# Performance work log

Measured on AMD Instinct MI355X. Metric: run time of the kernel, lower is better.

Reference implementation:

```python
import jax, jax.numpy as jnp
import numpy as np

N_NODES = 50000
N_EDGES = 800000
D_IN = 96
D_OUT = 96
K_ORDER = 3


def setup_inputs() -> dict:
    key = jax.random.key(0)
    k1, k2, k3, k4, k5 = jax.random.split(key, 5)
    rows = jax.random.randint(k1, (N_EDGES,), 0, N_NODES, dtype=jnp.int64 if jax.config.jax_enable_x64 else jnp.int32)
    cols = jax.random.randint(k2, (N_EDGES,), 0, N_NODES, dtype=jnp.int64 if jax.config.jax_enable_x64 else jnp.int32)
    vals = jax.random.uniform(k3, (N_EDGES,), dtype=jnp.float32) * (1.0 / 16.0)  # ~sym-normalized weights
    H = jax.random.normal(k4, (N_NODES, D_IN), dtype=jnp.float32)
    W = jax.random.normal(k5, (D_IN, D_OUT), dtype=jnp.float32) * (1.0 / np.sqrt(D_IN))
    bias = jnp.zeros((D_OUT,), dtype=jnp.float32)
    return {"rows": rows, "cols": cols, "vals": vals, "H": H, "W": W, "bias": bias}


def reference(rows, cols, vals, H, W, bias):
    n = H.shape[0]

    def spmm(X):  # L @ X via gather-multiply-scatter over COO edges
        return jax.ops.segment_sum(vals[:, None] * X[cols], rows, num_segments=n)

    def ln_mm(X):  # (2L - I) @ X
        return 2.0 * spmm(X) - X

    # k = 0 term: T_0 = H
    H_out = H @ W
    # k = 1 term: T_1 = (2L - I) H  (differentiable, as in torch code)
    T_prev = H
    T_curr = ln_mm(H)
    H_out = H_out + T_curr @ W
    # k >= 2: recurrence computed under no_grad in the original -> stop_gradient
    for _ in range(2, K_ORDER + 1):
        T_next = jax.lax.stop_gradient(2.0 * ln_mm(T_curr) - T_prev)
        H_out = H_out + T_next @ W
        T_prev, T_curr = T_curr, T_next
    return H_out + bias
```

## Files before the change

kernel.cpp:

```cpp
#include <hip/hip_runtime.h>
#include <hip/hip_fp16.h>

#define NN 50000
#define NE 800000
#define D  96
#define NB_SCAN 196
#define N4 (NN * D / 4)
#define CB4 ((N4 + 255) / 256)
#define WFRAG_BLKS 5

typedef unsigned int   uint32;
typedef unsigned short uint16;
typedef short  v8s __attribute__((ext_vector_type(8)));
typedef float  v4f __attribute__((ext_vector_type(4)));
typedef unsigned int v2u __attribute__((ext_vector_type(2)));
typedef unsigned int v4u __attribute__((ext_vector_type(4)));

__device__ inline uint16 f32_to_bf16(float f) {
    uint32 u = __float_as_uint(f);
    u += 0x7FFF + ((u >> 16) & 1);
    return (uint16)(u >> 16);
}

__device__ inline void u2f(v2u u, float& a, float& b, float& c, float& d) {
    a = __uint_as_float(u.x << 16);
    b = __uint_as_float(u.x & 0xFFFF0000u);
    c = __uint_as_float(u.y << 16);
    d = __uint_as_float(u.y & 0xFFFF0000u);
}

__device__ inline float f16_val(uint32 e) {
    __half_raw h; h.x = (uint16)(e >> 16);
    return __half2float(__half(h));
}

__device__ inline uint32 comb2(uint32 u1, uint32 u2, uint32 u3) {
    float a1 = __uint_as_float(u1 << 16), b1 = __uint_as_float(u1 & 0xFFFF0000u);
    float a2 = __uint_as_float(u2 << 16), b2 = __uint_as_float(u2 & 0xFFFF0000u);
    float a3 = __uint_as_float(u3 << 16), b3 = __uint_as_float(u3 & 0xFFFF0000u);
    float sa = 12.f * a1 - 40.f * a2 + 32.f * a3;
    float sb = 12.f * b1 - 40.f * b2 + 32.f * b3;
    return (uint32)f32_to_bf16(sa) | ((uint32)f32_to_bf16(sb) << 16);
}

__global__ void prep(const float4* __restrict__ H, ushort4* __restrict__ Hb,
                     const float* __restrict__ W, uint16* __restrict__ Wfrag,
                     int* __restrict__ counts) {
    int b = blockIdx.x;
    int t = threadIdx.x;
    if (b < CB4) {
        int i = b * 256 + t;
        if (i < N4) {
            float4 v = H[i];
            ushort4 o;
            o.x = f32_to_bf16(v.x); o.y = f32_to_bf16(v.y);
            o.z = f32_to_bf16(v.z); o.w = f32_to_bf16(v.w);
            Hb[i] = o;
        }
    } else if (b < CB4 + NB_SCAN) {
        int i = (b - CB4) * 256 + t;
        if (i < NN) counts[i] = 0;
    } else {
        int idx = (b - CB4 - NB_SCAN) * 256 + t;
        if (idx < 18 * 64) {
            int bt = idx >> 6, lane = idx & 63;
            int nt = bt / 3, kc = bt % 3;
            int col = nt * 16 + (lane & 15);
            int kbase = kc * 32 + (lane >> 4) * 8;
            uint16 tmp[8];
            #pragma unroll
            for (int j = 0; j < 8; ++j) tmp[j] = f32_to_bf16(W[(kbase + j) * D + col]);
            uint32* dst = (uint32*)(Wfrag + ((size_t)bt * 64 + lane) * 8);
            const uint32* src = (const uint32*)tmp;
            #pragma unroll
            for (int j = 0; j < 4; ++j) dst[j] = src[j];
        }
    }
}

__global__ void hist_slots(const int* __restrict__ rows, int* __restrict__ counts,
                           int* __restrict__ slot) {
    int e = blockIdx.x * blockDim.x + threadIdx.x;
    if (e < NE) slot[e] = atomicAdd(&counts[rows[e]], 1);
}

__global__ void scan_p1(const int* __restrict__ counts, int* __restrict__ partials) {
    __shared__ int red[256];
    int t = threadIdx.x;
    int i = blockIdx.x * 256 + t;
    red[t] = (i < NN) ? counts[i] : 0;
    __syncthreads();
    for (int off = 128; off > 0; off >>= 1) {
        if (t < off) red[t] += red[t + off];
        __syncthreads();
    }
    if (t == 0) partials[blockIdx.x] = red[0];
}

__global__ void scan_p23(const int* __restrict__ counts, const int* __restrict__ partials,
                         int* __restrict__ row_ptr) {
    __shared__ int pp[256];
    __shared__ int sh[256];
    int t = threadIdx.x;
    pp[t] = (t < NB_SCAN) ? partials[t] : 0;
    __syncthreads();
    for (int off = 1; off < 256; off <<= 1) {
        int u = (t >= off) ? pp[t - off] : 0;
        __syncthreads();
        pp[t] += u;
        __syncthreads();
    }
    int blk_off = (blockIdx.x == 0) ? 0 : pp[blockIdx.x - 1];
    int i = blockIdx.x * 256 + t;
    int v = (i < NN) ? counts[i] : 0;
    sh[t] = v;
    __syncthreads();
    for (int off = 1; off < 256; off <<= 1) {
        int u = (t >= off) ? sh[t - off] : 0;
        __syncthreads();
        sh[t] += u;
        __syncthreads();
    }
    int excl = sh[t] - v + blk_off;
    if (i < NN) row_ptr[i] = excl;
    if (i == NN - 1) row_ptr[NN] = excl + v;
}

__global__ void fill_edges(const int* __restrict__ rows, const int* __restrict__ cols,
                           const float* __restrict__ vals, const int* __restrict__ row_ptr,
                           const int* __restrict__ slot, uint32* __restrict__ edges) {
    int e = blockIdx.x * blockDim.x + threadIdx.x;
    if (e < NE) {
        int p = row_ptr[rows[e]] + slot[e];
        __half_raw hr = __half_raw(__float2half(vals[e]));
        edges[p] = (uint32)(cols[e] & 0xFFFF) | ((uint32)hr.x << 16);
    }
}

__global__ void spmm(const int* __restrict__ row_ptr, const uint32* __restrict__ edges,
                     const uint16* __restrict__ Xb, uint16* __restrict__ Yb) {
    int tid  = threadIdx.x;
    int lane = tid & 31;
    int g    = tid >> 5;
    int r = blockIdx.x * 8 + g;
    if (r >= NN) return;
    if (lane >= 24) return;

    const v2u* xbase = (const v2u*)Xb;

    float ax = 0.f, ay = 0.f, az = 0.f, aw = 0.f;

    int s = row_ptr[r];
    int e = row_ptr[r + 1];
    int i = s;
    for (; i + 7 < e; i += 8) {
        uint32 ee[8];
        #pragma unroll
        for (int j = 0; j < 8; ++j) ee[j] = edges[i + j];
        v2u xx[8];
        #pragma unroll
        for (int j = 0; j < 8; ++j)
            xx[j] = xbase[(size_t)(ee[j] & 0xFFFF) * 24 + lane];
        #pragma unroll
        for (int j = 0; j < 8; ++j) {
            float v = f16_val(ee[j]);
            float x0,x1,x2,x3;
            u2f(xx[j], x0,x1,x2,x3);
            ax += v*x0; ay += v*x1; az += v*x2; aw += v*x3;
        }
    }
    for (; i + 3 < e; i += 4) {
        uint32 ee[4];
        #pragma unroll
        for (int j = 0; j < 4; ++j) ee[j] = edges[i + j];
        v2u xx[4];
        #pragma unroll
        for (int j = 0; j < 4; ++j)
            xx[j] = xbase[(size_t)(ee[j] & 0xFFFF) * 24 + lane];
        #pragma unroll
        for (int j = 0; j < 4; ++j) {
            float v = f16_val(ee[j]);
            float x0,x1,x2,x3;
            u2f(xx[j], x0,x1,x2,x3);
            ax += v*x0; ay += v*x1; az += v*x2; aw += v*x3;
        }
    }
    for (; i < e; ++i) {
        uint32 e0 = edges[i];
        float v = f16_val(e0);
        v2u x = xbase[(size_t)(e0 & 0xFFFF) * 24 + lane];
        float x0,x1,x2,x3;
        u2f(x, x0,x1,x2,x3);
        ax += v*x0; ay += v*x1; az += v*x2; aw += v*x3;
    }

    v2u o;
    o.x = (uint32)f32_to_bf16(ax) | ((uint32)f32_to_bf16(ay) << 16);
    o.y = (uint32)f32_to_bf16(az) | ((uint32)f32_to_bf16(aw) << 16);
    __builtin_nontemporal_store(o, (v2u*)(Yb + (size_t)r * D) + lane);
}

__global__ void mfma_gemm(const uint16* __restrict__ U1, const uint16* __restrict__ U2,
                          const uint16* __restrict__ U3, const uint16* __restrict__ Wfrag,
                          const float* __restrict__ bias, float* __restrict__ out) {
    int tid   = threadIdx.x;
    int lane  = tid & 63;
    int wv    = blockIdx.x * (blockDim.x >> 6) + (tid >> 6);
    int nwv   = gridDim.x * (blockDim.x >> 6);
    int col   = lane & 15;
    int quad  = lane >> 4;

    v8s wf[6][3];
    #pragma unroll
    for (int nt = 0; nt < 6; ++nt)
        #pragma unroll
        for (int kc = 0; kc < 3; ++kc)
            wf[nt][kc] = ((const v8s*)Wfrag)[(nt * 3 + kc) * 64 + lane];

    float bi[6];
    #pragma unroll
    for (int nt = 0; nt < 6; ++nt) bi[nt] = bias[nt * 16 + col];

    for (int s = wv; s < NN / 16; s += nwv) {
        int r0 = s * 16;
        size_t base = (size_t)(r0 + col) * D + quad * 8;
        v8s a[3];
        #pragma unroll
        for (int kc = 0; kc < 3; ++kc) {
            v4u u1 = *(const v4u*)(U1 + base + kc * 32);
            v4u u2 = *(const v4u*)(U2 + base + kc * 32);
            v4u u3 = *(const v4u*)(U3 + base + kc * 32);
            v4u sres;
            #pragma unroll
            for (int j = 0; j < 4; ++j) sres[j] = comb2(u1[j], u2[j], u3[j]);
            a[kc] = __builtin_bit_cast(v8s, sres);
        }
        v4f acc[6];
        #pragma unroll
        for (int nt = 0; nt < 6; ++nt) {
            v4f c = {0.f, 0.f, 0.f, 0.f};
            c = __builtin_amdgcn_mfma_f32_16x16x32_bf16(a[0], wf[nt][0], c, 0, 0, 0);
            c = __builtin_amdgcn_mfma_f32_16x16x32_bf16(a[1], wf[nt][1], c, 0, 0, 0);
            c = __builtin_amdgcn_mfma_f32_16x16x32_bf16(a[2], wf[nt][2], c, 0, 0, 0);
            acc[nt] = c;
        }
        #pragma unroll
        for (int nt = 0; nt < 6; ++nt) {
            float* o = out + (size_t)(r0 + quad * 4) * D + nt * 16 + col;
            o[0 * D] = acc[nt][0] + bi[nt];
            o[1 * D] = acc[nt][1] + bi[nt];
            o[2 * D] = acc[nt][2] + bi[nt];
            o[3 * D] = acc[nt][3] + bi[nt];
        }
    }
}

extern "C" void kernel_launch(void* const* d_in, const int* in_sizes, int n_in,
                              void* d_out, int out_size, void* d_ws, size_t ws_size,
                              hipStream_t stream) {
    const int*   rows = (const int*)d_in[0];
    const int*   cols = (const int*)d_in[1];
    const float* vals = (const float*)d_in[2];
    const float* H    = (const float*)d_in[3];
    const float* W    = (const float*)d_in[4];
    const float* bias = (const float*)d_in[5];
    float* out = (float*)d_out;

    char* ws = (char*)d_ws;
    uint16* Hb       = (uint16*)ws;  ws += (size_t)NN * D * 2;
    uint16* U1b      = (uint16*)ws;  ws += (size_t)NN * D * 2;
    uint16* U2b      = (uint16*)ws;  ws += (size_t)NN * D * 2;
    uint16* U3b      = (uint16*)ws;  ws += (size_t)NN * D * 2;
    uint32* edges    = (uint32*)ws;  ws += (size_t)NE * 4;
    uint16* Wfrag    = (uint16*)ws;  ws += (size_t)18 * 64 * 8 * 2;
    int*    counts   = (int*)ws;     ws += (size_t)NN * 4;
    int*    row_ptr  = (int*)ws;     ws += (size_t)(NN + 1) * 4;
    int*    partials = (int*)ws;     ws += 256 * 4;
    int*    slot     = (int*)U2b;

    const int eb = (NE + 255) / 256;

    prep<<<CB4 + NB_SCAN + WFRAG_BLKS, 256, 0, stream>>>(
        (const float4*)H, (ushort4*)Hb, W, Wfrag, counts);
    hist_slots<<<eb, 256, 0, stream>>>(rows, counts, slot);
    scan_p1<<<NB_SCAN, 256, 0, stream>>>(counts, partials);
    scan_p23<<<NB_SCAN, 256, 0, stream>>>(counts, partials, row_ptr);
    fill_edges<<<eb, 256, 0, stream>>>(rows, cols, vals, row_ptr, slot, edges);

    const int sb = (NN + 7) / 8;

    spmm<<<sb, 256, 0, stream>>>(row_ptr, edges, Hb,  U1b);
    spmm<<<sb, 256, 0, stream>>>(row_ptr, edges, U1b, U2b);
    spmm<<<sb, 256, 0, stream>>>(row_ptr, edges, U2b, U3b);
    mfma_gemm<<<391, 256, 0, stream>>>(U1b, U2b, U3b, Wfrag, bias, out);
}
```

Measured before the change: 231.4 us.

## Split SpMM into 32-feature column slices to shrink gathered working set

```diff
diff --git a/kernel.cpp b/kernel.cpp
--- a/kernel.cpp
+++ b/kernel.cpp
@@ -20,13 +20,6 @@
     uint32 u = __float_as_uint(f);
     u += 0x7FFF + ((u >> 16) & 1);
     return (uint16)(u >> 16);
-}
-
-__device__ inline void u2f(v2u u, float& a, float& b, float& c, float& d) {
-    a = __uint_as_float(u.x << 16);
-    b = __uint_as_float(u.x & 0xFFFF0000u);
-    c = __uint_as_float(u.y << 16);
-    d = __uint_as_float(u.y & 0xFFFF0000u);
 }
 
 __device__ inline float f16_val(uint32 e) {
@@ -137,67 +130,57 @@
     }
 }
 
-__global__ void spmm(const int* __restrict__ row_ptr, const uint32* __restrict__ edges,
-                     const uint16* __restrict__ Xb, uint16* __restrict__ Yb) {
-    int tid  = threadIdx.x;
-    int lane = tid & 31;
-    int g    = tid >> 5;
-    int r = blockIdx.x * 8 + g;
-    if (r >= NN) return;
-    if (lane >= 24) return;
-
-    const v2u* xbase = (const v2u*)Xb;
-
-    float ax = 0.f, ay = 0.f, az = 0.f, aw = 0.f;
-
-    int s = row_ptr[r];
-    int e = row_ptr[r + 1];
+__global__ void spmm_slice(const int* __restrict__ row_ptr, const uint32* __restrict__ edges,
+                           const uint16* __restrict__ Xb, uint16* __restrict__ Yb,
+                           int slice) {
+    int tid = threadIdx.x;
+    int fl  = tid & 15;
+    int r   = blockIdx.x * 16 + (tid >> 4);
+    const uint16* xs = Xb + (size_t)slice * 32 + fl * 2;
+
+    float a0 = 0.f, a1 = 0.f;
+    int s = row_ptr[r], e = row_ptr[r + 1];
     int i = s;
     for (; i + 7 < e; i += 8) {
         uint32 ee[8];
         #pragma unroll
         for (int j = 0; j < 8; ++j) ee[j] = edges[i + j];
-        v2u xx[8];
+        uint32 xx[8];
         #pragma unroll
         for (int j = 0; j < 8; ++j)
-            xx[j] = xbase[(size_t)(ee[j] & 0xFFFF) * 24 + lane];
+            xx[j] = *(const uint32*)(xs + (size_t)(ee[j] & 0xFFFF) * D);
         #pragma unroll
         for (int j = 0; j < 8; ++j) {
             float v = f16_val(ee[j]);
-            float x0,x1,x2,x3;
-            u2f(xx[j], x0,x1,x2,x3);
-            ax += v*x0; ay += v*x1; az += v*x2; aw += v*x3;
+            a0 += v * __uint_as_float(xx[j] << 16);
+            a1 += v * __uint_as_float(xx[j] & 0xFFFF0000u);
         }
     }
     for (; i + 3 < e; i += 4) {
         uint32 ee[4];
         #pragma unroll
         for (int j = 0; j < 4; ++j) ee[j] = edges[i + j];
-        v2u xx[4];
+        uint32 xx[4];
         #pragma unroll
         for (int j = 0; j < 4; ++j)
-            xx[j] = xbase[(size_t)(ee[j] & 0xFFFF) * 24 + lane];
+            xx[j] = *(const uint32*)(xs + (size_t)(ee[j] & 0xFFFF) * D);
         #pragma unroll
         for (int j = 0; j < 4; ++j) {
             float v = f16_val(ee[j]);
-            float x0,x1,x2,x3;
-            u2f(xx[j], x0,x1,x2,x3);
-            ax += v*x0; ay += v*x1; az += v*x2; aw += v*x3;
+            a0 += v * __uint_as_float(xx[j] << 16);
+            a1 += v * __uint_as_float(xx[j] & 0xFFFF0000u);
         }
     }
     for (; i < e; ++i) {
         uint32 e0 = edges[i];
         float v = f16_val(e0);
-        v2u x = xbase[(size_t)(e0 & 0xFFFF) * 24 + lane];
-        float x0,x1,x2,x3;
-        u2f(x, x0,x1,x2,x3);
-        ax += v*x0; ay += v*x1; az += v*x2; aw += v*x3;
-    }
-
-    v2u o;
-    o.x = (uint32)f32_to_bf16(ax) | ((uint32)f32_to_bf16(ay) << 16);
-    o.y = (uint32)f32_to_bf16(az) | ((uint32)f32_to_bf16(aw) << 16);
-    __builtin_nontemporal_store(o, (v2u*)(Yb + (size_t)r * D) + lane);
+        uint32 x = *(const uint32*)(xs + (size_t)(e0 & 0xFFFF) * D);
+        a0 += v * __uint_as_float(x << 16);
+        a1 += v * __uint_as_float(x & 0xFFFF0000u);
+    }
+
+    uint32 o = (uint32)f32_to_bf16(a0) | ((uint32)f32_to_bf16(a1) << 16);
+    *(uint32*)(Yb + (size_t)r * D + slice * 32 + fl * 2) = o;
 }
 
 __global__ void mfma_gemm(const uint16* __restrict__ U1, const uint16* __restrict__ U2,
@@ -287,10 +270,12 @@
     scan_p23<<<NB_SCAN, 256, 0, stream>>>(counts, partials, row_ptr);
     fill_edges<<<eb, 256, 0, stream>>>(rows, cols, vals, row_ptr, slot, edges);
 
-    const int sb = (NN + 7) / 8;
-
-    spmm<<<sb, 256, 0, stream>>>(row_ptr, edges, Hb,  U1b);
-    spmm<<<sb, 256, 0, stream>>>(row_ptr, edges, U1b, U2b);
-    spmm<<<sb, 256, 0, stream>>>(row_ptr, edges, U2b, U3b);
+    const int sb = NN / 16;
+
+    for (int s = 0; s < 3; ++s) {
+        spmm_slice<<<sb, 256, 0, stream>>>(row_ptr, edges, Hb,  U1b, s);
+        spmm_slice<<<sb, 256, 0, stream>>>(row_ptr, edges, U1b, U2b, s);
+        spmm_slice<<<sb, 256, 0, stream>>>(row_ptr, edges, U2b, U3b, s);
+    }
     mfma_gemm<<<391, 256, 0, stream>>>(U1b, U2b, U3b, Wfrag, bias, out);
 }
```

Measured after the change: 287.0 us. 24.0% more time.

## Pad CSR rows to multiples of eight for vectorized tail-free SpMM

Applied to the files above, without the earlier changes.

```diff
diff --git a/kernel.cpp b/kernel.cpp
--- a/kernel.cpp
+++ b/kernel.cpp
@@ -8,6 +8,9 @@
 #define N4 (NN * D / 4)
 #define CB4 ((N4 + 255) / 256)
 #define WFRAG_BLKS 5
+#define EMAX (NE + 8 * NN)
+#define EZ4  (EMAX / 4)
+#define EZB  ((EZ4 + 255) / 256)
 
 typedef unsigned int   uint32;
 typedef unsigned short uint16;
@@ -45,7 +48,7 @@
 
 __global__ void prep(const float4* __restrict__ H, ushort4* __restrict__ Hb,
                      const float* __restrict__ W, uint16* __restrict__ Wfrag,
-                     int* __restrict__ counts) {
+                     int* __restrict__ counts, v4u* __restrict__ edges4) {
     int b = blockIdx.x;
     int t = threadIdx.x;
     if (b < CB4) {
@@ -60,7 +63,7 @@
     } else if (b < CB4 + NB_SCAN) {
         int i = (b - CB4) * 256 + t;
         if (i < NN) counts[i] = 0;
-    } else {
+    } else if (b < CB4 + NB_SCAN + WFRAG_BLKS) {
         int idx = (b - CB4 - NB_SCAN) * 256 + t;
         if (idx < 18 * 64) {
             int bt = idx >> 6, lane = idx & 63;
@@ -75,6 +78,9 @@
             #pragma unroll
             for (int j = 0; j < 4; ++j) dst[j] = src[j];
         }
+    } else {
+        int i = (b - CB4 - NB_SCAN - WFRAG_BLKS) * 256 + t;
+        if (i < EZ4) edges4[i] = (v4u){0u, 0u, 0u, 0u};
     }
 }
 
@@ -88,7 +94,7 @@
     __shared__ int red[256];
     int t = threadIdx.x;
     int i = blockIdx.x * 256 + t;
-    red[t] = (i < NN) ? counts[i] : 0;
+    red[t] = (i < NN) ? ((counts[i] + 7) & ~7) : 0;
     __syncthreads();
     for (int off = 128; off > 0; off >>= 1) {
         if (t < off) red[t] += red[t + off];
@@ -112,7 +118,7 @@
     }
     int blk_off = (blockIdx.x == 0) ? 0 : pp[blockIdx.x - 1];
     int i = blockIdx.x * 256 + t;
-    int v = (i < NN) ? counts[i] : 0;
+    int v = (i < NN) ? ((counts[i] + 7) & ~7) : 0;
     sh[t] = v;
     __syncthreads();
     for (int off = 1; off < 256; off <<= 1) {
@@ -149,14 +155,12 @@
     const v2u* xbase = (const v2u*)Xb;
 
     float ax = 0.f, ay = 0.f, az = 0.f, aw = 0.f;
-
     int s = row_ptr[r];
     int e = row_ptr[r + 1];
-    int i = s;
-    for (; i + 7 < e; i += 8) {
-        uint32 ee[8];
-        #pragma unroll
-        for (int j = 0; j < 8; ++j) ee[j] = edges[i + j];
+    for (int i = s; i < e; i += 8) {
+        v4u ea = *(const v4u*)(edges + i);
+        v4u eb = *(const v4u*)(edges + i + 4);
+        uint32 ee[8] = {ea.x, ea.y, ea.z, ea.w, eb.x, eb.y, eb.z, eb.w};
         v2u xx[8];
         #pragma unroll
         for (int j = 0; j < 8; ++j)
@@ -168,30 +172,6 @@
             u2f(xx[j], x0,x1,x2,x3);
             ax += v*x0; ay += v*x1; az += v*x2; aw += v*x3;
         }
-    }
-    for (; i + 3 < e; i += 4) {
-        uint32 ee[4];
-        #pragma unroll
-        for (int j = 0; j < 4; ++j) ee[j] = edges[i + j];
-        v2u xx[4];
-        #pragma unroll
-        for (int j = 0; j < 4; ++j)
-            xx[j] = xbase[(size_t)(ee[j] & 0xFFFF) * 24 + lane];
-        #pragma unroll
-        for (int j = 0; j < 4; ++j) {
-            float v = f16_val(ee[j]);
-            float x0,x1,x2,x3;
-            u2f(xx[j], x0,x1,x2,x3);
-            ax += v*x0; ay += v*x1; az += v*x2; aw += v*x3;
-        }
-    }
-    for (; i < e; ++i) {
-        uint32 e0 = edges[i];
-        float v = f16_val(e0);
-        v2u x = xbase[(size_t)(e0 & 0xFFFF) * 24 + lane];
-        float x0,x1,x2,x3;
-        u2f(x, x0,x1,x2,x3);
-        ax += v*x0; ay += v*x1; az += v*x2; aw += v*x3;
     }
 
     v2u o;
@@ -247,10 +227,10 @@
         #pragma unroll
         for (int nt = 0; nt < 6; ++nt) {
             float* o = out + (size_t)(r0 + quad * 4) * D + nt * 16 + col;
-            o[0 * D] = acc[nt][0] + bi[nt];
-            o[1 * D] = acc[nt][1] + bi[nt];
-            o[2 * D] = acc[nt][2] + bi[nt];
-            o[3 * D] = acc[nt][3] + bi[nt];
+            __builtin_nontemporal_store(acc[nt][0] + bi[nt], o + 0 * D);
+            __builtin_nontemporal_store(acc[nt][1] + bi[nt], o + 1 * D);
+            __builtin_nontemporal_store(acc[nt][2] + bi[nt], o + 2 * D);
+            __builtin_nontemporal_store(acc[nt][3] + bi[nt], o + 3 * D);
         }
     }
 }
@@ -271,7 +251,7 @@
     uint16* U1b      = (uint16*)ws;  ws += (size_t)NN * D * 2;
     uint16* U2b      = (uint16*)ws;  ws += (size_t)NN * D * 2;
     uint16* U3b      = (uint16*)ws;  ws += (size_t)NN * D * 2;
-    uint32* edges    = (uint32*)ws;  ws += (size_t)NE * 4;
+    uint32* edges    = (uint32*)ws;  ws += (size_t)EMAX * 4;
     uint16* Wfrag    = (uint16*)ws;  ws += (size_t)18 * 64 * 8 * 2;
     int*    counts   = (int*)ws;     ws += (size_t)NN * 4;
     int*    row_ptr  = (int*)ws;     ws += (size_t)(NN + 1) * 4;
@@ -280,8 +260,8 @@
 
     const int eb = (NE + 255) / 256;
 
-    prep<<<CB4 + NB_SCAN + WFRAG_BLKS, 256, 0, stream>>>(
-        (const float4*)H, (ushort4*)Hb, W, Wfrag, counts);
+    prep<<<CB4 + NB_SCAN + WFRAG_BLKS + EZB, 256, 0, stream>>>(
+        (const float4*)H, (ushort4*)Hb, W, Wfrag, counts, (v4u*)edges);
     hist_slots<<<eb, 256, 0, stream>>>(rows, counts, slot);
     scan_p1<<<NB_SCAN, 256, 0, stream>>>(counts, partials);
     scan_p23<<<NB_SCAN, 256, 0, stream>>>(counts, partials, row_ptr);
@@ -292,5 +272,5 @@
     spmm<<<sb, 256, 0, stream>>>(row_ptr, edges, Hb,  U1b);
     spmm<<<sb, 256, 0, stream>>>(row_ptr, edges, U1b, U2b);
     spmm<<<sb, 256, 0, stream>>>(row_ptr, edges, U2b, U3b);
-    mfma_gemm<<<391, 256, 0, stream>>>(U1b, U2b, U3b, Wfrag, bias, out);
-}
+    mfma_gemm<<<782, 256, 0, stream>>>(U1b, U2b, U3b, Wfrag, bias, out);
+}
```

Measured after the change: 230.9 us. No clear change (-0.2%).
